# Kernel tuning notes

Measured on AMD Instinct MI355X. Metric: run time of the kernel, lower is better.

## Reference

```python
import jax, jax.numpy as jnp
import numpy as np

G, L, H = 8, 16, 768  # num_global_heads, num_local_heads, hidden_dim
D = H // G            # head_size = 96
B, N = 16, 512


def setup_inputs() -> dict:
    key = jax.random.key(0)
    ks = jax.random.split(key, 10)
    inp = {
        "x": jax.random.normal(ks[0], (B, N, H), dtype=jnp.float32),
        "encoding_bias": jax.random.normal(ks[1], (B, N, N), dtype=jnp.float32),
        # noise injected into global attention scores (randn_like(g_k))
        "eps": jax.random.normal(ks[2], (B, G, N, N), dtype=jnp.float32),
        # params: torch Linear stored here as (in, out) so y = x @ W
        "Wq": jax.random.normal(ks[3], (H, H), dtype=jnp.float32) / np.sqrt(H),
        "Wk": jax.random.normal(ks[4], (H, H), dtype=jnp.float32) / np.sqrt(H),
        "Wv": jax.random.normal(ks[5], (H, L * D), dtype=jnp.float32) / np.sqrt(H),
        "bv": jax.random.normal(ks[6], (L * D,), dtype=jnp.float32) * 0.01,
        "sigma": 0.1 * jnp.ones((G,), dtype=jnp.float32),
        "p": jax.random.normal(ks[7], (G, L), dtype=jnp.float32),
        "Wout": jax.random.normal(ks[8], (L * D, H), dtype=jnp.float32) / np.sqrt(L * D),
    }
    return inp


def mish(x):
    return x * jnp.tanh(jax.nn.softplus(x))


def reference(x, encoding_bias, eps, Wq, Wk, Wv, bv, sigma, p, Wout):
    b, n, h = x.shape
    g, l = p.shape
    d = h // g
    scale = h ** (-0.5)
    bias = encoding_bias[:, None, :, :]  # (b,1,n,n)

    q = (x @ Wq).reshape(b, n, g, d)
    k = (x @ Wk).reshape(b, n, g, d)
    v = (x @ Wv + bv).reshape(b, n, l, d)

    g_k = jnp.einsum('bngd,bmgd->bgnm', q, k)            # global QK^T
    pad_mask = jnp.all(g_k == 0, axis=-1)                # (b,g,n) padded rows
    a = g_k + (sigma ** 2)[None, :, None, None] * eps    # noise injection
    a = jnp.where(pad_mask[..., None], 0.0, a)

    a = jnp.einsum('bgnm,gl->blnm', a, p)                # head admixture
    pad_mask2 = jnp.all(a == 0, axis=-1)                 # (b,l,n)
    a = jnp.where(pad_mask2[..., None], -jnp.inf, mish(a))

    a = a * scale + bias
    a = jax.nn.softmax(a, axis=-1)
    a = jnp.nan_to_num(a)                                # all -inf rows -> 0

    o = jnp.einsum('blnm,bmld->bnld', a, v)              # (b,n,l,d); dropout = eval identity
    return o.reshape(b, n, l * d) @ Wout
```

## Files before the change

kernel.cpp:

```cpp
#include <hip/hip_runtime.h>
#include <stdint.h>
#include <stddef.h>

typedef __attribute__((ext_vector_type(8))) short bf16x8;
typedef __attribute__((ext_vector_type(4))) short s16x4;
typedef __attribute__((ext_vector_type(4))) float f32x4;

__device__ __forceinline__ short f2bf(float x) {
  uint32_t u = __builtin_bit_cast(uint32_t, x);
  u += 0x7fffu + ((u >> 16) & 1u);
  return (short)(u >> 16);
}

__device__ __forceinline__ void gload16(const short* g, short* l) {
  __builtin_amdgcn_global_load_lds(
      (const __attribute__((address_space(1))) void*)g,
      (__attribute__((address_space(3))) void*)l, 16, 0, 0);
}

#define PB 16
#define PN 512
#define PH 768
#define PG 8
#define PD 96
#define PL 16
#define PLD 1536
#define PC 3072

__global__ void transpose_bf16_k(const float* __restrict__ src, short* __restrict__ dst,
                                 int R, int C) {
  __shared__ float tile[32][33];
  int c0 = blockIdx.x * 32, r0 = blockIdx.y * 32;
  int tx = threadIdx.x;
  int ty = threadIdx.y;
  for (int i = 0; i < 4; i++) {
    int r = r0 + ty + i * 8;
    tile[ty + i * 8][tx] = src[(size_t)r * C + c0 + tx];
  }
  __syncthreads();
  for (int i = 0; i < 4; i++) {
    int c = c0 + ty + i * 8;
    dst[(size_t)c * R + r0 + tx] = f2bf(tile[tx][ty + i * 8]);
  }
}

__global__ __launch_bounds__(256) void convert_bf16_k(const float* __restrict__ src,
                                                      short* __restrict__ dst) {
  int i = (blockIdx.x * 256 + threadIdx.x) * 4;
  float4 v = *(const float4*)(src + i);
  s16x4 o = { f2bf(v.x), f2bf(v.y), f2bf(v.z), f2bf(v.w) };
  *(s16x4*)(dst + i) = o;
}

__global__ __launch_bounds__(256) void gemm_qkv_k(
    const short* __restrict__ Xb, const short* __restrict__ Wt,
    const float* __restrict__ bv, short* __restrict__ Cb) {
  __shared__ short As[128 * 32];
  __shared__ short Bs[128 * 32];
  int n0 = blockIdx.x * 128;
  int m0 = blockIdx.y * 128;
  int tid = threadIdx.x;
  int wave = tid >> 6, lane = tid & 63, quad = lane >> 4, l16 = lane & 15;
  int wm = wave & 1, wn = wave >> 1;

  f32x4 acc[4][4] = {};

  for (int k0 = 0; k0 < PH; k0 += 32) {
#pragma unroll
    for (int t = 0; t < 2; t++) {
      int rb = (wave * 2 + t) * 16;
      gload16(Xb + (size_t)(m0 + rb + (lane >> 2)) * PH + k0 + (lane & 3) * 8,
              &As[rb * 32]);
      gload16(Wt + (size_t)(n0 + rb + (lane >> 2)) * PH + k0 + (lane & 3) * 8,
              &Bs[rb * 32]);
    }
    __syncthreads();
    bf16x8 af[4], bfv[4];
#pragma unroll
    for (int i = 0; i < 4; i++)
      af[i] = *(bf16x8*)&As[(wm * 64 + i * 16 + l16) * 32 + quad * 8];
#pragma unroll
    for (int j = 0; j < 4; j++)
      bfv[j] = *(bf16x8*)&Bs[(wn * 64 + j * 16 + l16) * 32 + quad * 8];
#pragma unroll
    for (int i = 0; i < 4; i++)
#pragma unroll
      for (int j = 0; j < 4; j++)
        acc[i][j] = __builtin_amdgcn_mfma_f32_16x16x32_bf16(af[i], bfv[j], acc[i][j], 0, 0, 0);
    __syncthreads();
  }

  bool isv = (n0 >= 2 * PH);
  float bvr[4] = {0.f, 0.f, 0.f, 0.f};
  if (isv)
#pragma unroll
    for (int j = 0; j < 4; j++)
      bvr[j] = bv[n0 + wn * 64 + j * 16 + l16 - 2 * PH];

#pragma unroll
  for (int i = 0; i < 4; i++) {
    int rowb = m0 + wm * 64 + i * 16 + quad * 4;
#pragma unroll
    for (int j = 0; j < 4; j++) {
      int col = n0 + wn * 64 + j * 16 + l16;
#pragma unroll
      for (int r = 0; r < 4; r++)
        Cb[(size_t)(rowb + r) * PC + col] = f2bf(acc[i][j][r] + bvr[j]);
    }
  }
}

__global__ __launch_bounds__(256) void vtrans2_k(const short* __restrict__ Cb,
                                                 short* __restrict__ vbt) {
  __shared__ short tile[32][36];
  int b = blockIdx.z;
  int ld0 = blockIdx.y * 32;
  int n0 = blockIdx.x * 32;
  int t = threadIdx.x;
  int r = t >> 3, c = (t & 7) * 4;
  *(uint2*)&tile[r][c] =
      *(const uint2*)(Cb + ((size_t)(b * PN) + n0 + r) * PC + 2 * PH + ld0 + c);
  __syncthreads();
  s16x4 o = { tile[c + 0][r], tile[c + 1][r], tile[c + 2][r], tile[c + 3][r] };
  *(s16x4*)(vbt + ((size_t)(b * PLD) + ld0 + r) * PN + n0 + c) = o;
}

#define SB_STR 68
#define PB_STR 72
__global__ __launch_bounds__(256, 2) void fused_attn_k(
    const short* __restrict__ Cb, const float* __restrict__ eps,
    const float* __restrict__ ebias, const float* __restrict__ sigma,
    const float* __restrict__ p, const short* __restrict__ vbt,
    short* __restrict__ ob) {
  __shared__ __align__(16) float sb[PG][16 * SB_STR];
  __shared__ __align__(16) short pb[PL][16 * PB_STR];
  __shared__ float pLs[PG][PL];
  __shared__ float sg2s[PG];

  int n0 = blockIdx.x * 16;
  int b = blockIdx.y;
  int tid = threadIdx.x;
  int wave = tid >> 6, lane = tid & 63, quad = lane >> 4, l16 = lane & 15;

  if (tid < PG * PL) pLs[tid >> 4][tid & 15] = p[tid];
  if (tid < PG) { float s = sigma[tid]; sg2s[tid] = s * s; }
  __syncthreads();
  float sg2r[PG];
#pragma unroll
  for (int g = 0; g < PG; g++) sg2r[g] = sg2s[g];

  const float scale = 0.03608439182435161f;

  bf16x8 aq[2][3];
#pragma unroll
  for (int gg = 0; gg < 2; gg++) {
    int g = wave * 2 + gg;
    const short* qg = Cb + ((size_t)(b * PN) + n0 + l16) * PC + g * PD;
#pragma unroll
    for (int ks = 0; ks < 3; ks++)
      aq[gg][ks] = *(const bf16x8*)(qg + ks * 32 + quad * 8);
  }

  bf16x8 onesf;
#pragma unroll
  for (int j = 0; j < 8; j++) onesf[j] = (short)0x3F80;

  f32x4 oacc[4][6] = {};
  f32x4 sacc[4] = {};

  float er[4][PG];
  float br[4];
#pragma unroll
  for (int s = 0; s < 4; s++) {
    int n = wave + 4 * s;
#pragma unroll
    for (int g = 0; g < PG; g++)
      er[s][g] = eps[((size_t)(b * PG + g) * PN + n0 + n) * PN + lane];
    br[s] = ebias[((size_t)b * PN + n0 + n) * PN + lane];
  }

  for (int mt = 0; mt < 8; mt++) {
    int m0 = mt * 64;
#pragma unroll
    for (int gg = 0; gg < 2; gg++) {
      int g = wave * 2 + gg;
      const short* kg = Cb + ((size_t)(b * PN) + m0) * PC + PH + g * PD;
#pragma unroll
      for (int ms = 0; ms < 4; ms++) {
        f32x4 acc = {};
#pragma unroll
        for (int ks = 0; ks < 3; ks++) {
          bf16x8 bk = *(const bf16x8*)(kg + (size_t)(ms * 16 + l16) * PC + ks * 32 + quad * 8);
          acc = __builtin_amdgcn_mfma_f32_16x16x32_bf16(aq[gg][ks], bk, acc, 0, 0, 0);
        }
#pragma unroll
        for (int r = 0; r < 4; r++)
          sb[g][(quad * 4 + r) * SB_STR + ms * 16 + l16] = acc[r];
      }
    }
    __syncthreads();
    float2 sv[2][PG];
#pragma unroll
    for (int sp = 0; sp < 2; sp++) {
      int na = wave + 4 * (2 * sp), nb_ = wave + 4 * (2 * sp + 1);
#pragma unroll
      for (int g = 0; g < PG; g++) {
        sv[sp][g].x = sb[g][na * SB_STR + lane] + sg2r[g] * er[2 * sp][g];
        sv[sp][g].y = sb[g][nb_ * SB_STR + lane] + sg2r[g] * er[2 * sp + 1][g];
      }
    }
    float bias2[2][2] = {{br[0], br[1]}, {br[2], br[3]}};
    {
      int m0n = (mt < 7) ? (m0 + 64) : m0;
#pragma unroll
      for (int s = 0; s < 4; s++) {
        int n = wave + 4 * s;
#pragma unroll
        for (int g = 0; g < PG; g++)
          er[s][g] = eps[((size_t)(b * PG + g) * PN + n0 + n) * PN + m0n + lane];
        br[s] = ebias[((size_t)b * PN + n0 + n) * PN + m0n + lane];
      }
    }
    for (int l = 0; l < PL; l++) {
      float2 a2[2] = {{0.f, 0.f}, {0.f, 0.f}};
#pragma unroll
      for (int g = 0; g < PG; g++) {
        float pv = pLs[g][l];
        a2[0].x += sv[0][g].x * pv; a2[0].y += sv[0][g].y * pv;
        a2[1].x += sv[1][g].x * pv; a2[1].y += sv[1][g].y * pv;
      }
#pragma unroll
      for (int sp = 0; sp < 2; sp++) {
#pragma unroll
        for (int h = 0; h < 2; h++) {
          float a = h ? a2[sp].y : a2[sp].x;
          float ex = __expf(a);
          float t = 1.f + ex;
          float r2 = t * t;
          float mi = (a > 20.f) ? a : a * (r2 - 1.f) * __builtin_amdgcn_rcpf(r2 + 1.f);
          float e = __expf(mi * scale + bias2[sp][h]);
          pb[l][(wave + 4 * (2 * sp + h)) * PB_STR + lane] = f2bf(e);
        }
      }
    }
    __syncthreads();
#pragma unroll
    for (int li = 0; li < 4; li++) {
      int l = wave * 4 + li;
      bf16x8 af0 = *(bf16x8*)&pb[l][l16 * PB_STR + 0 + quad * 8];
      bf16x8 af1 = *(bf16x8*)&pb[l][l16 * PB_STR + 32 + quad * 8];
      const short* vb = vbt + ((size_t)(b * PL + l) * PD) * PN + m0;
#pragma unroll
      for (int dt = 0; dt < 6; dt++) {
        bf16x8 b0 = *(const bf16x8*)(vb + (size_t)(dt * 16 + l16) * PN + quad * 8);
        bf16x8 b1 = *(const bf16x8*)(vb + (size_t)(dt * 16 + l16) * PN + 32 + quad * 8);
        oacc[li][dt] = __builtin_amdgcn_mfma_f32_16x16x32_bf16(af0, b0, oacc[li][dt], 0, 0, 0);
        oacc[li][dt] = __builtin_amdgcn_mfma_f32_16x16x32_bf16(af1, b1, oacc[li][dt], 0, 0, 0);
      }
      sacc[li] = __builtin_amdgcn_mfma_f32_16x16x32_bf16(af0, onesf, sacc[li], 0, 0, 0);
      sacc[li] = __builtin_amdgcn_mfma_f32_16x16x32_bf16(af1, onesf, sacc[li], 0, 0, 0);
    }
  }

#pragma unroll
  for (int li = 0; li < 4; li++) {
    int l = wave * 4 + li;
#pragma unroll
    for (int r = 0; r < 4; r++) {
      int n = quad * 4 + r;
      float inv = __builtin_amdgcn_rcpf(sacc[li][r]);
#pragma unroll
      for (int dt = 0; dt < 6; dt++) {
        float o = oacc[li][dt][r] * inv;
        ob[((size_t)(b * PN) + n0 + n) * PLD + l * PD + dt * 16 + l16] = f2bf(o);
      }
    }
  }
}

__global__ __launch_bounds__(256) void gemm_out_k(
    const short* __restrict__ A, const short* __restrict__ Bt,
    float* __restrict__ out) {
  __shared__ short As[128 * 32];
  __shared__ short Bs[128 * 32];
  int n0 = blockIdx.x * 128;
  int m0 = blockIdx.y * 128;
  int tid = threadIdx.x;
  int wave = tid >> 6, lane = tid & 63, quad = lane >> 4, l16 = lane & 15;
  int wm = wave & 1, wn = wave >> 1;
  f32x4 acc[4][4] = {};
  for (int k0 = 0; k0 < PLD; k0 += 32) {
#pragma unroll
    for (int t = 0; t < 2; t++) {
      int rb = (wave * 2 + t) * 16;
      gload16(A + (size_t)(m0 + rb + (lane >> 2)) * PLD + k0 + (lane & 3) * 8,
              &As[rb * 32]);
      gload16(Bt + (size_t)(n0 + rb + (lane >> 2)) * PLD + k0 + (lane & 3) * 8,
              &Bs[rb * 32]);
    }
    __syncthreads();
    bf16x8 af[4], bfv[4];
#pragma unroll
    for (int i = 0; i < 4; i++)
      af[i] = *(bf16x8*)&As[(wm * 64 + i * 16 + l16) * 32 + quad * 8];
#pragma unroll
    for (int j = 0; j < 4; j++)
      bfv[j] = *(bf16x8*)&Bs[(wn * 64 + j * 16 + l16) * 32 + quad * 8];
#pragma unroll
    for (int i = 0; i < 4; i++)
#pragma unroll
      for (int j = 0; j < 4; j++)
        acc[i][j] = __builtin_amdgcn_mfma_f32_16x16x32_bf16(af[i], bfv[j], acc[i][j], 0, 0, 0);
    __syncthreads();
  }
#pragma unroll
  for (int i = 0; i < 4; i++) {
    int rowb = m0 + wm * 64 + i * 16 + quad * 4;
#pragma unroll
    for (int j = 0; j < 4; j++) {
      int col = n0 + wn * 64 + j * 16 + l16;
#pragma unroll
      for (int r = 0; r < 4; r++)
        out[(size_t)(rowb + r) * PH + col] = acc[i][j][r];
    }
  }
}

extern "C" void kernel_launch(void* const* d_in, const int* in_sizes, int n_in,
                              void* d_out, int out_size, void* d_ws, size_t ws_size,
                              hipStream_t stream) {
  (void)in_sizes; (void)n_in; (void)out_size; (void)ws_size;
  const float* x     = (const float*)d_in[0];
  const float* ebias = (const float*)d_in[1];
  const float* eps   = (const float*)d_in[2];
  const float* Wq    = (const float*)d_in[3];
  const float* Wk    = (const float*)d_in[4];
  const float* Wv    = (const float*)d_in[5];
  const float* bv    = (const float*)d_in[6];
  const float* sigma = (const float*)d_in[7];
  const float* p     = (const float*)d_in[8];
  const float* Wout  = (const float*)d_in[9];
  float* out = (float*)d_out;

  char* ws = (char*)d_ws;
  short* xb     = (short*)(ws + 0);
  short* wqkv_t = (short*)(ws + 12582912);
  short* wout_t = (short*)(ws + 17301504);
  short* Cb     = (short*)(ws + 19660800);
  short* vbt    = (short*)(ws + 69992448);
  short* ob     = (short*)(ws + 95158272);

  dim3 tb(32, 8);
  transpose_bf16_k<<<dim3(24, 24), tb, 0, stream>>>(Wq, wqkv_t, PH, PH);
  transpose_bf16_k<<<dim3(24, 24), tb, 0, stream>>>(Wk, wqkv_t + 768 * 768, PH, PH);
  transpose_bf16_k<<<dim3(48, 24), tb, 0, stream>>>(Wv, wqkv_t + 1536 * 768, PH, PLD);
  transpose_bf16_k<<<dim3(24, 48), tb, 0, stream>>>(Wout, wout_t, PLD, PH);
  convert_bf16_k<<<dim3(6144), 256, 0, stream>>>(x, xb);

  gemm_qkv_k<<<dim3(24, 64), 256, 0, stream>>>(xb, wqkv_t, bv, Cb);
  vtrans2_k<<<dim3(16, 48, 16), 256, 0, stream>>>(Cb, vbt);
  fused_attn_k<<<dim3(32, 16), 256, 0, stream>>>(Cb, eps, ebias, sigma, p, vbt, ob);
  gemm_out_k<<<dim3(6, 64), 256, 0, stream>>>(ob, wout_t, out);
}
```

Measured before the change: 570.8 us.

## Keep QK scores in registers and double-buffer probability LDS to drop a barrier

Repartitions the QK^T stage so each wave computes all 8 global heads for its own 16 key columns, instead of 2 heads over all 64 columns. The scores therefore stay in MFMA accumulator registers rather than going through the sb shared buffer, which removes one LDS round trip and one __syncthreads per key tile. The probability buffer becomes double-buffered so a single barrier per iteration is enough. In exchange, Q fragments are reloaded from global memory on every tile instead of being held in registers, the l loop is fully unrolled (more register pressure under launch_bounds(256,2)), and the prefetch on the last tile is skipped.

```diff
diff --git a/kernel.cpp b/kernel.cpp
--- a/kernel.cpp
+++ b/kernel.cpp
@@ -125,22 +125,21 @@
   *(s16x4*)(vbt + ((size_t)(b * PLD) + ld0 + r) * PN + n0 + c) = o;
 }
 
-#define SB_STR 68
-#define PB_STR 72
+#define PBSTR 68
+#define PBROW (16 * PBSTR)
 __global__ __launch_bounds__(256, 2) void fused_attn_k(
     const short* __restrict__ Cb, const float* __restrict__ eps,
     const float* __restrict__ ebias, const float* __restrict__ sigma,
     const float* __restrict__ p, const short* __restrict__ vbt,
     short* __restrict__ ob) {
-  __shared__ __align__(16) float sb[PG][16 * SB_STR];
-  __shared__ __align__(16) short pb[PL][16 * PB_STR];
+  __shared__ __align__(16) short pbuf[2][PL * PBROW];
   __shared__ float pLs[PG][PL];
   __shared__ float sg2s[PG];
 
   int n0 = blockIdx.x * 16;
   int b = blockIdx.y;
   int tid = threadIdx.x;
-  int wave = tid >> 6, lane = tid & 63, quad = lane >> 4, l16 = lane & 15;
+  int w = tid >> 6, lane = tid & 63, quad = lane >> 4, l16 = lane & 15;
 
   if (tid < PG * PL) pLs[tid >> 4][tid & 15] = p[tid];
   if (tid < PG) { float s = sigma[tid]; sg2s[tid] = s * s; }
@@ -151,16 +150,6 @@
 
   const float scale = 0.03608439182435161f;
 
-  bf16x8 aq[2][3];
-#pragma unroll
-  for (int gg = 0; gg < 2; gg++) {
-    int g = wave * 2 + gg;
-    const short* qg = Cb + ((size_t)(b * PN) + n0 + l16) * PC + g * PD;
-#pragma unroll
-    for (int ks = 0; ks < 3; ks++)
-      aq[gg][ks] = *(const bf16x8*)(qg + ks * 32 + quad * 8);
-  }
-
   bf16x8 onesf;
 #pragma unroll
   for (int j = 0; j < 8; j++) onesf[j] = (short)0x3F80;
@@ -168,59 +157,57 @@
   f32x4 oacc[4][6] = {};
   f32x4 sacc[4] = {};
 
+  const short* qbase = Cb + ((size_t)(b * PN) + n0 + l16) * PC;
+
   float er[4][PG];
   float br[4];
-#pragma unroll
-  for (int s = 0; s < 4; s++) {
-    int n = wave + 4 * s;
-#pragma unroll
-    for (int g = 0; g < PG; g++)
-      er[s][g] = eps[((size_t)(b * PG + g) * PN + n0 + n) * PN + lane];
-    br[s] = ebias[((size_t)b * PN + n0 + n) * PN + lane];
+  {
+    int ms = w * 16 + l16;
+#pragma unroll
+    for (int r = 0; r < 4; r++) {
+#pragma unroll
+      for (int g = 0; g < PG; g++)
+        er[r][g] = eps[((size_t)(b * PG + g) * PN + n0 + quad * 4 + r) * PN + ms];
+      br[r] = ebias[((size_t)b * PN + n0 + quad * 4 + r) * PN + ms];
+    }
   }
 
   for (int mt = 0; mt < 8; mt++) {
     int m0 = mt * 64;
-#pragma unroll
-    for (int gg = 0; gg < 2; gg++) {
-      int g = wave * 2 + gg;
-      const short* kg = Cb + ((size_t)(b * PN) + m0) * PC + PH + g * PD;
-#pragma unroll
-      for (int ms = 0; ms < 4; ms++) {
-        f32x4 acc = {};
-#pragma unroll
-        for (int ks = 0; ks < 3; ks++) {
-          bf16x8 bk = *(const bf16x8*)(kg + (size_t)(ms * 16 + l16) * PC + ks * 32 + quad * 8);
-          acc = __builtin_amdgcn_mfma_f32_16x16x32_bf16(aq[gg][ks], bk, acc, 0, 0, 0);
-        }
-#pragma unroll
-        for (int r = 0; r < 4; r++)
-          sb[g][(quad * 4 + r) * SB_STR + ms * 16 + l16] = acc[r];
-      }
-    }
-    __syncthreads();
+    short* pw = pbuf[mt & 1];
+    f32x4 csc[PG];
+    const short* kbase = Cb + ((size_t)(b * PN) + m0 + w * 16 + l16) * PC + PH;
+#pragma unroll
+    for (int g = 0; g < PG; g++) {
+      f32x4 acc = {};
+#pragma unroll
+      for (int ks = 0; ks < 3; ks++) {
+        bf16x8 aq = *(const bf16x8*)(qbase + g * PD + ks * 32 + quad * 8);
+        bf16x8 bk = *(const bf16x8*)(kbase + g * PD + ks * 32 + quad * 8);
+        acc = __builtin_amdgcn_mfma_f32_16x16x32_bf16(aq, bk, acc, 0, 0, 0);
+      }
+      csc[g] = acc;
+    }
     float2 sv[2][PG];
 #pragma unroll
-    for (int sp = 0; sp < 2; sp++) {
-      int na = wave + 4 * (2 * sp), nb_ = wave + 4 * (2 * sp + 1);
+    for (int sp = 0; sp < 2; sp++)
 #pragma unroll
       for (int g = 0; g < PG; g++) {
-        sv[sp][g].x = sb[g][na * SB_STR + lane] + sg2r[g] * er[2 * sp][g];
-        sv[sp][g].y = sb[g][nb_ * SB_STR + lane] + sg2r[g] * er[2 * sp + 1][g];
-      }
-    }
-    float bias2[2][2] = {{br[0], br[1]}, {br[2], br[3]}};
-    {
-      int m0n = (mt < 7) ? (m0 + 64) : m0;
-#pragma unroll
-      for (int s = 0; s < 4; s++) {
-        int n = wave + 4 * s;
+        sv[sp][g].x = csc[g][2 * sp]     + sg2r[g] * er[2 * sp][g];
+        sv[sp][g].y = csc[g][2 * sp + 1] + sg2r[g] * er[2 * sp + 1][g];
+      }
+    float bb[4] = {br[0], br[1], br[2], br[3]};
+    if (mt < 7) {
+      int ms = m0 + 64 + w * 16 + l16;
+#pragma unroll
+      for (int r = 0; r < 4; r++) {
 #pragma unroll
         for (int g = 0; g < PG; g++)
-          er[s][g] = eps[((size_t)(b * PG + g) * PN + n0 + n) * PN + m0n + lane];
-        br[s] = ebias[((size_t)b * PN + n0 + n) * PN + m0n + lane];
-      }
-    }
+          er[r][g] = eps[((size_t)(b * PG + g) * PN + n0 + quad * 4 + r) * PN + ms];
+        br[r] = ebias[((size_t)b * PN + n0 + quad * 4 + r) * PN + ms];
+      }
+    }
+#pragma unroll
     for (int l = 0; l < PL; l++) {
       float2 a2[2] = {{0.f, 0.f}, {0.f, 0.f}};
 #pragma unroll
@@ -238,17 +225,18 @@
           float t = 1.f + ex;
           float r2 = t * t;
           float mi = (a > 20.f) ? a : a * (r2 - 1.f) * __builtin_amdgcn_rcpf(r2 + 1.f);
-          float e = __expf(mi * scale + bias2[sp][h]);
-          pb[l][(wave + 4 * (2 * sp + h)) * PB_STR + lane] = f2bf(e);
+          float e = __expf(mi * scale + bb[2 * sp + h]);
+          int nr = quad * 4 + 2 * sp + h;
+          pw[l * PBROW + nr * PBSTR + w * 16 + l16] = f2bf(e);
         }
       }
     }
     __syncthreads();
 #pragma unroll
     for (int li = 0; li < 4; li++) {
-      int l = wave * 4 + li;
-      bf16x8 af0 = *(bf16x8*)&pb[l][l16 * PB_STR + 0 + quad * 8];
-      bf16x8 af1 = *(bf16x8*)&pb[l][l16 * PB_STR + 32 + quad * 8];
+      int l = w * 4 + li;
+      bf16x8 af0 = *(bf16x8*)&pw[l * PBROW + l16 * PBSTR + quad * 8];
+      bf16x8 af1 = *(bf16x8*)&pw[l * PBROW + l16 * PBSTR + 32 + quad * 8];
       const short* vb = vbt + ((size_t)(b * PL + l) * PD) * PN + m0;
 #pragma unroll
       for (int dt = 0; dt < 6; dt++) {
@@ -264,7 +252,7 @@
 
 #pragma unroll
   for (int li = 0; li < 4; li++) {
-    int l = wave * 4 + li;
+    int l = w * 4 + li;
 #pragma unroll
     for (int r = 0; r < 4; r++) {
       int n = quad * 4 + r;
```

New measurement: 574.6 us. About the same (+0.7%).
